# Kernel tuning notes

Hardware: AMD Instinct MI355X
Metric: run time of the kernel (lower is better)

## Reference

```python
import jax, jax.numpy as jnp
import numpy as np

D_IN = 6      # raw node feature dim (self_attn_init first arg)
D_INIT = 16   # init encoding dim (self_attn_init second arg)
D_CAT = 22    # 6 + 16 (self_attn_enc first arg)
D_ENC = 64    # encoding dim (self_attn_enc second arg / gated_aggr_attn)
N = 1024      # number of nodes in node_cloud


def setup_inputs() -> dict:
    key = jax.random.key(0)
    ks = jax.random.split(key, 8)
    return {
        "node_cloud": jax.random.normal(ks[0], (N, D_IN), jnp.float32),
        "Wq_i": jax.random.normal(ks[1], (D_IN, D_INIT), jnp.float32) / np.sqrt(D_IN),
        "Wk_i": jax.random.normal(ks[2], (D_IN, D_INIT), jnp.float32) / np.sqrt(D_IN),
        "Wv_i": jax.random.normal(ks[3], (D_IN, D_INIT), jnp.float32) / np.sqrt(D_IN),
        "Wq_e": jax.random.normal(ks[4], (D_IN, D_ENC), jnp.float32) / np.sqrt(D_IN),
        "Wk_e": jax.random.normal(ks[5], (D_CAT, D_ENC), jnp.float32) / np.sqrt(D_CAT),
        "Wv_e": jax.random.normal(ks[6], (D_CAT, D_ENC), jnp.float32) / np.sqrt(D_CAT),
        "wg": jax.random.normal(ks[7], (D_ENC,), jnp.float32) / np.sqrt(D_ENC),
        "bg": jnp.zeros((), jnp.float32),
    }


def reference(node_cloud, Wq_i, Wk_i, Wv_i, Wq_e, Wk_e, Wv_e, wg, bg):
    # Stage 1: self_attn_init, batched over all C=N centres at once.
    # Per centre c: attend over every node, per-node 16-d encoding.
    Q_i = node_cloud @ Wq_i                     # [C, 16] (one query per centre)
    K_i = node_cloud @ Wk_i                     # [N, 16]
    V_i = node_cloud @ Wv_i                     # [N, 16]
    scores_i = (Q_i @ K_i.T) / np.sqrt(D_INIT)  # [C, N]
    a_i = jax.nn.softmax(scores_i, axis=-1)     # [C, N]
    nce_init = a_i[:, :, None] * V_i[None]      # [C, N, 16]

    # Stage 2: self_attn_enc on concat(raw node feats, init encodings).
    x = jnp.concatenate(
        [jnp.broadcast_to(node_cloud[None], (N, N, D_IN)), nce_init], axis=-1
    )                                            # [C, N, 22]
    Q_e = node_cloud @ Wq_e                      # [C, 64]
    K_e = jnp.einsum("cnf,fd->cnd", x, Wk_e)     # [C, N, 64]
    V_e = jnp.einsum("cnf,fd->cnd", x, Wv_e)     # [C, N, 64]
    scores_e = jnp.einsum("cnd,cd->cn", K_e, Q_e) / np.sqrt(D_ENC)  # [C, N]
    a_e = jax.nn.softmax(scores_e, axis=-1)      # [C, N]
    enc = a_e[:, :, None] * V_e                  # [C, N, 64]

    # Stage 3: gated_aggr_attn over the node axis -> one 64-vector per centre.
    g = jax.nn.sigmoid(enc @ wg + bg)            # [C, N]
    out = jnp.einsum("cn,cnd->cd", g, enc)       # [C, 64]
    return out
```

## Files before the change

kernel.cpp:

```cpp
#include <hip/hip_runtime.h>
#include <math.h>

#define NN 1024
#define DIN 6
#define DI 16
#define DE 64
#define DCAT 22
#define GC 4
#define NTC 512
#define NWAVE (NTC/64)

#define OFF_XT    0
#define OFF_VIT   (OFF_XT + 6*NN)
#define OFF_GR    (OFF_VIT + 16*NN)
#define OFF_GV    (OFF_GR + NN)
#define OFF_QREC  (OFF_GV + NN)

__device__ __forceinline__ float wave_sum(float v) {
    int t;
    t = __builtin_amdgcn_update_dpp(0, __float_as_int(v), 0x111, 0xf, 0xf, true); v += __int_as_float(t);
    t = __builtin_amdgcn_update_dpp(0, __float_as_int(v), 0x112, 0xf, 0xf, true); v += __int_as_float(t);
    t = __builtin_amdgcn_update_dpp(0, __float_as_int(v), 0x114, 0xf, 0xf, true); v += __int_as_float(t);
    t = __builtin_amdgcn_update_dpp(0, __float_as_int(v), 0x118, 0xf, 0xf, true); v += __int_as_float(t);
    t = __builtin_amdgcn_update_dpp(0, __float_as_int(v), 0x142, 0xf, 0xf, true); v += __int_as_float(t);
    t = __builtin_amdgcn_update_dpp(0, __float_as_int(v), 0x143, 0xf, 0xf, true); v += __int_as_float(t);
    return v;
}

__global__ __launch_bounds__(256) void nce_pre(
    const float* __restrict__ nc,
    const float* __restrict__ Wq_i, const float* __restrict__ Wk_i,
    const float* __restrict__ Wv_i, const float* __restrict__ Wq_e,
    const float* __restrict__ Wk_e, const float* __restrict__ Wv_e,
    const float* __restrict__ wg, float* __restrict__ ws)
{
    __shared__ float s_wqi[96], s_wki[96], s_wvi[96];
    __shared__ float s_wqe[384], s_wke[1408], s_wve[1408], s_wg[64];
    __shared__ float s_t[4][64], s_vi[4][16], s_qi[4][16];
    const int tid = threadIdx.x, w = tid >> 6, lane = tid & 63;

    for (int i = tid; i < 96; i += 256) { s_wqi[i]=Wq_i[i]; s_wki[i]=Wk_i[i]; s_wvi[i]=Wv_i[i]; }
    for (int i = tid; i < 384; i += 256) s_wqe[i] = Wq_e[i];
    for (int i = tid; i < 1408; i += 256) { s_wke[i]=Wk_e[i]; s_wve[i]=Wv_e[i]; }
    if (tid < 64) s_wg[tid] = wg[tid];
    __syncthreads();

    const int n = blockIdx.x*4 + w;
    float x[6];
    #pragma unroll
    for (int f = 0; f < 6; ++f) x[f] = nc[n*6 + f];

    float t = 0.f, vr = 0.f;
    #pragma unroll
    for (int f = 0; f < 6; ++f) {
        t  += x[f]*s_wqe[f*64 + lane];
        vr += x[f]*s_wve[f*64 + lane];
    }
    s_t[w][lane] = t;
    if (lane < 16) {
        float vi = 0.f, qi = 0.f;
        #pragma unroll
        for (int f = 0; f < 6; ++f) {
            vi += x[f]*s_wvi[f*16 + lane];
            qi += x[f]*s_wqi[f*16 + lane];
        }
        s_vi[w][lane] = vi; s_qi[w][lane] = qi;
        ws[OFF_VIT + lane*NN + n] = vi;
    }
    __syncthreads();

    float vv = 0.f;
    #pragma unroll
    for (int j = 0; j < 16; ++j) vv += s_vi[w][j]*s_wve[(6+j)*64 + lane];

    float gr = wave_sum(vr*s_wg[lane]);
    float gv = wave_sum(vv*s_wg[lane]);
    if (lane == 63) { ws[OFF_GR + n] = gr; ws[OFF_GV + n] = gv; }

    if (lane < 6) {
        ws[OFF_XT + lane*NN + n] = x[lane];
        float a = 0.f;
        #pragma unroll
        for (int j = 0; j < 16; ++j) a += s_wki[lane*16 + j]*s_qi[w][j];
        ws[OFF_QREC + lane*NN + n] = a*0.25f;
    }
    if (lane < 22) {
        const float* row = s_wke + lane*64;
        float a = 0.f;
        for (int d = 0; d < 64; ++d) a += row[d]*s_t[w][d];
        const int krow = (lane < 6) ? (8 + lane) : (10 + lane);
        ws[OFF_QREC + krow*NN + n] = a*0.125f;
    }
}

__global__ __launch_bounds__(NTC, 2) void nce_centre(
    const float* __restrict__ ws, const float* __restrict__ bgp,
    const float* __restrict__ Wv_e, float* __restrict__ out)
{
    __shared__ float  s_wve[DCAT*DE];
    __shared__ float  s_q[GC][32];
    __shared__ float4 s_red1[NWAVE], s_red2[NWAVE];
    __shared__ float4 s_acc[NWAVE][22];
    __shared__ float  s_fin[22*4];

    const int tid = threadIdx.x, wave = tid >> 6, lane = tid & 63;
    const int c0 = blockIdx.x*GC;

    for (int i = tid; i < DCAT*DE; i += NTC) s_wve[i] = Wv_e[i];
    if (tid < GC*32) s_q[tid >> 5][tid & 31] = ws[OFF_QREC + (tid & 31)*NN + c0 + (tid >> 5)];

    const int nA = tid, nB = tid + NTC;
    float xA[6], xB[6], viA[16], viB[16];
    #pragma unroll
    for (int f = 0; f < 6; ++f) { xA[f] = ws[OFF_XT + f*NN + nA]; xB[f] = ws[OFF_XT + f*NN + nB]; }
    #pragma unroll
    for (int j = 0; j < 16; ++j) { viA[j] = ws[OFF_VIT + j*NN + nA]; viB[j] = ws[OFF_VIT + j*NN + nB]; }
    const float grA = ws[OFF_GR + nA], grB = ws[OFF_GR + nB];
    const float gvA = ws[OFF_GV + nA], gvB = ws[OFF_GV + nB];
    const float bg = *bgp;
    __syncthreads();

    float aiA[GC], aiB[GC];
    {
        float r[GC];
        #pragma unroll
        for (int c = 0; c < GC; ++c) {
            const float* q = s_q[c];
            float sA = 0.f, sB = 0.f;
            #pragma unroll
            for (int f = 0; f < 6; ++f) { sA += q[f]*xA[f]; sB += q[f]*xB[f]; }
            aiA[c] = __expf(sA); aiB[c] = __expf(sB);
            r[c] = aiA[c] + aiB[c];
        }
        float r0 = wave_sum(r[0]), r1 = wave_sum(r[1]), r2 = wave_sum(r[2]), r3 = wave_sum(r[3]);
        if (lane == 63) s_red1[wave] = make_float4(r0, r1, r2, r3);
    }
    __syncthreads();
    {
        float4 dd = s_red1[0];
        #pragma unroll
        for (int w2 = 1; w2 < NWAVE; ++w2) {
            float4 t = s_red1[w2]; dd.x += t.x; dd.y += t.y; dd.z += t.z; dd.w += t.w;
        }
        float den[GC] = {dd.x, dd.y, dd.z, dd.w};
        #pragma unroll
        for (int c = 0; c < GC; ++c) { float inv = 1.f/den[c]; aiA[c] *= inv; aiB[c] *= inv; }
    }

    float w1A[GC], w2A[GC], w1B[GC], w2B[GC];
    {
        float eA[GC], eB[GC];
        #pragma unroll
        for (int c = 0; c < GC; ++c) {
            const float* q = s_q[c];
            float uA = 0.f, uB = 0.f, vA = 0.f, vB = 0.f;
            #pragma unroll
            for (int f = 0; f < 6; ++f) { uA += q[8+f]*xA[f]; uB += q[8+f]*xB[f]; }
            #pragma unroll
            for (int j = 0; j < 16; ++j) { vA += q[16+j]*viA[j]; vB += q[16+j]*viB[j]; }
            eA[c] = __expf(uA + aiA[c]*vA);
            eB[c] = __expf(uB + aiB[c]*vB);
        }
        float s0 = wave_sum(eA[0]+eB[0]), s1 = wave_sum(eA[1]+eB[1]);
        float s2 = wave_sum(eA[2]+eB[2]), s3 = wave_sum(eA[3]+eB[3]);
        if (lane == 63) s_red2[wave] = make_float4(s0, s1, s2, s3);
        __syncthreads();
        float4 dd = s_red2[0];
        #pragma unroll
        for (int w2 = 1; w2 < NWAVE; ++w2) {
            float4 t = s_red2[w2]; dd.x += t.x; dd.y += t.y; dd.z += t.z; dd.w += t.w;
        }
        float den2[GC] = {dd.x, dd.y, dd.z, dd.w};
        #pragma unroll
        for (int c = 0; c < GC; ++c) {
            float inv = 1.f/den2[c];
            float aeA = eA[c]*inv, aeB = eB[c]*inv;
            float preA = aeA*(grA + aiA[c]*gvA) + bg;
            float preB = aeB*(grB + aiB[c]*gvB) + bg;
            float gA = 1.f/(1.f + __expf(-preA));
            float gB = 1.f/(1.f + __expf(-preB));
            w1A[c] = gA*aeA; w2A[c] = w1A[c]*aiA[c];
            w1B[c] = gB*aeB; w2B[c] = w1B[c]*aiB[c];
        }
    }

    #pragma unroll
    for (int f = 0; f < 6; ++f) {
        float a0 = wave_sum(w1A[0]*xA[f] + w1B[0]*xB[f]);
        float a1 = wave_sum(w1A[1]*xA[f] + w1B[1]*xB[f]);
        float a2 = wave_sum(w1A[2]*xA[f] + w1B[2]*xB[f]);
        float a3 = wave_sum(w1A[3]*xA[f] + w1B[3]*xB[f]);
        if (lane == 63) s_acc[wave][f] = make_float4(a0, a1, a2, a3);
    }
    #pragma unroll
    for (int j = 0; j < 16; ++j) {
        float a0 = wave_sum(w2A[0]*viA[j] + w2B[0]*viB[j]);
        float a1 = wave_sum(w2A[1]*viA[j] + w2B[1]*viB[j]);
        float a2 = wave_sum(w2A[2]*viA[j] + w2B[2]*viB[j]);
        float a3 = wave_sum(w2A[3]*viA[j] + w2B[3]*viB[j]);
        if (lane == 63) s_acc[wave][6+j] = make_float4(a0, a1, a2, a3);
    }
    __syncthreads();
    if (tid < 88) {
        const int k = tid >> 2, c = tid & 3;
        const float* af = (const float*)s_acc;
        float a = 0.f;
        #pragma unroll
        for (int w2 = 0; w2 < NWAVE; ++w2) a += af[(w2*22 + k)*4 + c];
        s_fin[k*4 + c] = a;
    }
    __syncthreads();

    if (tid < GC*DE) {
        const int c = tid >> 6, d = tid & 63;
        float o = 0.f;
        #pragma unroll
        for (int k = 0; k < DCAT; ++k) o += s_fin[k*4 + c]*s_wve[k*64 + d];
        out[(c0 + c)*DE + d] = o;
    }
}

extern "C" void kernel_launch(void* const* d_in, const int* in_sizes, int n_in,
                              void* d_out, int out_size, void* d_ws, size_t ws_size,
                              hipStream_t stream)
{
    const float* nc   = (const float*)d_in[0];
    const float* Wq_i = (const float*)d_in[1];
    const float* Wk_i = (const float*)d_in[2];
    const float* Wv_i = (const float*)d_in[3];
    const float* Wq_e = (const float*)d_in[4];
    const float* Wk_e = (const float*)d_in[5];
    const float* Wv_e = (const float*)d_in[6];
    const float* wg   = (const float*)d_in[7];
    const float* bg   = (const float*)d_in[8];
    float* out = (float*)d_out;
    float* ws  = (float*)d_ws;

    nce_pre<<<NN/4, 256, 0, stream>>>(nc, Wq_i, Wk_i, Wv_i, Wq_e, Wk_e, Wv_e, wg, ws);
    nce_centre<<<NN/GC, NTC, 0, stream>>>(ws, bg, Wv_e, out);
}
```

Baseline: 19.33 us.

## Fold weight products into small matrices in single-block setup; halve centres per block

The setup kernel now runs as a single 1024-thread block. It first builds the folded 6x22 matrix Wq_e·Wk_eᵀ, the 6x6 matrix Wq_i·Wk_iᵀ and the vector Wv_e·wg, then computes each node's per-node projections with a few small dot products instead of per-wave 64-wide reductions. The centre kernel handles 2 centres per block instead of 4, which doubles the grid to 512 blocks, and raises the occupancy hint to 4 blocks per CU. This cuts the redundant weight-matrix work in the prologue and spreads the main kernel across more CUs. In exchange, the setup kernel runs on one CU, and every centre block reloads the shared weights and node data twice as often in total.

```diff
diff --git a/kernel.cpp b/kernel.cpp
--- a/kernel.cpp
+++ b/kernel.cpp
@@ -2,19 +2,18 @@
 #include <math.h>
 
 #define NN 1024
-#define DIN 6
-#define DI 16
 #define DE 64
 #define DCAT 22
-#define GC 4
+#define GC 2
 #define NTC 512
 #define NWAVE (NTC/64)
-
-#define OFF_XT    0
-#define OFF_VIT   (OFF_XT + 6*NN)
-#define OFF_GR    (OFF_VIT + 16*NN)
-#define OFF_GV    (OFF_GR + NN)
-#define OFF_QREC  (OFF_GV + NN)
+#define NBLK (NN/GC)
+
+#define OFF_XT   0
+#define OFF_VIT  (OFF_XT + 6*NN)
+#define OFF_GR   (OFF_VIT + 16*NN)
+#define OFF_GV   (OFF_GR + NN)
+#define OFF_QREC (OFF_GV + NN)
 
 __device__ __forceinline__ float wave_sum(float v) {
     int t;
@@ -27,7 +26,7 @@
     return v;
 }
 
-__global__ __launch_bounds__(256) void nce_pre(
+__global__ __launch_bounds__(1024) void nce_setup(
     const float* __restrict__ nc,
     const float* __restrict__ Wq_i, const float* __restrict__ Wk_i,
     const float* __restrict__ Wv_i, const float* __restrict__ Wq_e,
@@ -36,72 +35,83 @@
 {
     __shared__ float s_wqi[96], s_wki[96], s_wvi[96];
     __shared__ float s_wqe[384], s_wke[1408], s_wve[1408], s_wg[64];
-    __shared__ float s_t[4][64], s_vi[4][16], s_qi[4][16];
-    const int tid = threadIdx.x, w = tid >> 6, lane = tid & 63;
-
-    for (int i = tid; i < 96; i += 256) { s_wqi[i]=Wq_i[i]; s_wki[i]=Wk_i[i]; s_wvi[i]=Wv_i[i]; }
-    for (int i = tid; i < 384; i += 256) s_wqe[i] = Wq_e[i];
-    for (int i = tid; i < 1408; i += 256) { s_wke[i]=Wk_e[i]; s_wve[i]=Wv_e[i]; }
-    if (tid < 64) s_wg[tid] = wg[tid];
-    __syncthreads();
-
-    const int n = blockIdx.x*4 + w;
+    __shared__ float s_M[6*DCAT], s_Mi[36], s_u[DCAT];
+    const int tid = threadIdx.x;
+
+    if (tid < 96) { s_wqi[tid]=Wq_i[tid]; s_wki[tid]=Wk_i[tid]; s_wvi[tid]=Wv_i[tid]; }
+    { int t = tid - 128; if (t >= 0 && t < 384) s_wqe[t] = Wq_e[t]; }
+    { int t = tid - 512; if (t >= 0 && t < 64)  s_wg[t]  = wg[t]; }
+    for (int i = tid; i < 1408; i += 1024) { s_wke[i]=Wk_e[i]; s_wve[i]=Wv_e[i]; }
+    __syncthreads();
+
+    if (tid < 132) {
+        const int f = tid % 6, k = tid / 6;
+        float a = 0.f;
+        #pragma unroll
+        for (int d = 0; d < 64; ++d) a += s_wqe[f*64+d]*s_wke[k*64+d];
+        s_M[f*DCAT+k] = a * 0.125f;
+    } else if (tid < 168) {
+        const int t = tid - 132, g = t % 6, f = t / 6;
+        float a = 0.f;
+        #pragma unroll
+        for (int j = 0; j < 16; ++j) a += s_wqi[g*16+j]*s_wki[f*16+j];
+        s_Mi[g*6+f] = a * 0.25f;
+    } else if (tid < 190) {
+        const int k = tid - 168;
+        float a = 0.f;
+        #pragma unroll
+        for (int d = 0; d < 64; ++d) a += s_wve[k*64+d]*s_wg[d];
+        s_u[k] = a;
+    }
+    __syncthreads();
+
+    const int n = tid;
     float x[6];
     #pragma unroll
-    for (int f = 0; f < 6; ++f) x[f] = nc[n*6 + f];
-
-    float t = 0.f, vr = 0.f;
+    for (int f = 0; f < 6; ++f) { x[f] = nc[n*6 + f]; ws[OFF_XT + f*NN + n] = x[f]; }
+
+    float vi[16];
+    #pragma unroll
+    for (int j = 0; j < 16; ++j) {
+        float a = 0.f;
+        #pragma unroll
+        for (int f = 0; f < 6; ++f) a += x[f]*s_wvi[f*16+j];
+        vi[j] = a;
+        ws[OFF_VIT + j*NN + n] = a;
+    }
+    float gr = 0.f, gv = 0.f;
+    #pragma unroll
+    for (int f = 0; f < 6; ++f)  gr += x[f]*s_u[f];
+    #pragma unroll
+    for (int j = 0; j < 16; ++j) gv += vi[j]*s_u[6+j];
+    ws[OFF_GR + n] = gr;
+    ws[OFF_GV + n] = gv;
+
     #pragma unroll
     for (int f = 0; f < 6; ++f) {
-        t  += x[f]*s_wqe[f*64 + lane];
-        vr += x[f]*s_wve[f*64 + lane];
-    }
-    s_t[w][lane] = t;
-    if (lane < 16) {
-        float vi = 0.f, qi = 0.f;
-        #pragma unroll
-        for (int f = 0; f < 6; ++f) {
-            vi += x[f]*s_wvi[f*16 + lane];
-            qi += x[f]*s_wqi[f*16 + lane];
-        }
-        s_vi[w][lane] = vi; s_qi[w][lane] = qi;
-        ws[OFF_VIT + lane*NN + n] = vi;
-    }
-    __syncthreads();
-
-    float vv = 0.f;
-    #pragma unroll
-    for (int j = 0; j < 16; ++j) vv += s_vi[w][j]*s_wve[(6+j)*64 + lane];
-
-    float gr = wave_sum(vr*s_wg[lane]);
-    float gv = wave_sum(vv*s_wg[lane]);
-    if (lane == 63) { ws[OFF_GR + n] = gr; ws[OFF_GV + n] = gv; }
-
-    if (lane < 6) {
-        ws[OFF_XT + lane*NN + n] = x[lane];
-        float a = 0.f;
-        #pragma unroll
-        for (int j = 0; j < 16; ++j) a += s_wki[lane*16 + j]*s_qi[w][j];
-        ws[OFF_QREC + lane*NN + n] = a*0.25f;
-    }
-    if (lane < 22) {
-        const float* row = s_wke + lane*64;
-        float a = 0.f;
-        for (int d = 0; d < 64; ++d) a += row[d]*s_t[w][d];
-        const int krow = (lane < 6) ? (8 + lane) : (10 + lane);
-        ws[OFF_QREC + krow*NN + n] = a*0.125f;
-    }
-}
-
-__global__ __launch_bounds__(NTC, 2) void nce_centre(
+        float a = 0.f;
+        #pragma unroll
+        for (int g = 0; g < 6; ++g) a += x[g]*s_Mi[g*6+f];
+        ws[OFF_QREC + f*NN + n] = a;
+    }
+    #pragma unroll
+    for (int k = 0; k < DCAT; ++k) {
+        float a = 0.f;
+        #pragma unroll
+        for (int f = 0; f < 6; ++f) a += x[f]*s_M[f*DCAT+k];
+        ws[OFF_QREC + ((k < 6) ? (8+k) : (10+k))*NN + n] = a;
+    }
+}
+
+__global__ __launch_bounds__(NTC, 4) void nce_centre(
     const float* __restrict__ ws, const float* __restrict__ bgp,
     const float* __restrict__ Wv_e, float* __restrict__ out)
 {
     __shared__ float  s_wve[DCAT*DE];
     __shared__ float  s_q[GC][32];
-    __shared__ float4 s_red1[NWAVE], s_red2[NWAVE];
-    __shared__ float4 s_acc[NWAVE][22];
-    __shared__ float  s_fin[22*4];
+    __shared__ float2 s_red1[NWAVE], s_red2[NWAVE];
+    __shared__ float2 s_acc[NWAVE][DCAT];
+    __shared__ float  s_fin[DCAT*GC];
 
     const int tid = threadIdx.x, wave = tid >> 6, lane = tid & 63;
     const int c0 = blockIdx.x*GC;
@@ -121,30 +131,26 @@
     __syncthreads();
 
     float aiA[GC], aiB[GC];
+    #pragma unroll
+    for (int c = 0; c < GC; ++c) {
+        const float* q = s_q[c];
+        float sA = 0.f, sB = 0.f;
+        #pragma unroll
+        for (int f = 0; f < 6; ++f) { sA += q[f]*xA[f]; sB += q[f]*xB[f]; }
+        aiA[c] = __expf(sA); aiB[c] = __expf(sB);
+    }
     {
-        float r[GC];
-        #pragma unroll
-        for (int c = 0; c < GC; ++c) {
-            const float* q = s_q[c];
-            float sA = 0.f, sB = 0.f;
-            #pragma unroll
-            for (int f = 0; f < 6; ++f) { sA += q[f]*xA[f]; sB += q[f]*xB[f]; }
-            aiA[c] = __expf(sA); aiB[c] = __expf(sB);
-            r[c] = aiA[c] + aiB[c];
-        }
-        float r0 = wave_sum(r[0]), r1 = wave_sum(r[1]), r2 = wave_sum(r[2]), r3 = wave_sum(r[3]);
-        if (lane == 63) s_red1[wave] = make_float4(r0, r1, r2, r3);
+        float r0 = wave_sum(aiA[0]+aiB[0]);
+        float r1 = wave_sum(aiA[1]+aiB[1]);
+        if (lane == 63) s_red1[wave] = make_float2(r0, r1);
     }
     __syncthreads();
     {
-        float4 dd = s_red1[0];
-        #pragma unroll
-        for (int w2 = 1; w2 < NWAVE; ++w2) {
-            float4 t = s_red1[w2]; dd.x += t.x; dd.y += t.y; dd.z += t.z; dd.w += t.w;
-        }
-        float den[GC] = {dd.x, dd.y, dd.z, dd.w};
-        #pragma unroll
-        for (int c = 0; c < GC; ++c) { float inv = 1.f/den[c]; aiA[c] *= inv; aiB[c] *= inv; }
+        float2 dd = s_red1[0];
+        #pragma unroll
+        for (int w2 = 1; w2 < NWAVE; ++w2) { float2 t = s_red1[w2]; dd.x += t.x; dd.y += t.y; }
+        float inv0 = 1.f/dd.x, inv1 = 1.f/dd.y;
+        aiA[0] *= inv0; aiB[0] *= inv0; aiA[1] *= inv1; aiB[1] *= inv1;
     }
 
     float w1A[GC], w2A[GC], w1B[GC], w2B[GC];
@@ -161,19 +167,17 @@
             eA[c] = __expf(uA + aiA[c]*vA);
             eB[c] = __expf(uB + aiB[c]*vB);
         }
-        float s0 = wave_sum(eA[0]+eB[0]), s1 = wave_sum(eA[1]+eB[1]);
-        float s2 = wave_sum(eA[2]+eB[2]), s3 = wave_sum(eA[3]+eB[3]);
-        if (lane == 63) s_red2[wave] = make_float4(s0, s1, s2, s3);
+        float s0 = wave_sum(eA[0]+eB[0]);
+        float s1 = wave_sum(eA[1]+eB[1]);
+        if (lane == 63) s_red2[wave] = make_float2(s0, s1);
         __syncthreads();
-        float4 dd = s_red2[0];
-        #pragma unroll
-        for (int w2 = 1; w2 < NWAVE; ++w2) {
-            float4 t = s_red2[w2]; dd.x += t.x; dd.y += t.y; dd.z += t.z; dd.w += t.w;
-        }
-        float den2[GC] = {dd.x, dd.y, dd.z, dd.w};
+        float2 dd = s_red2[0];
+        #pragma unroll
+        for (int w2 = 1; w2 < NWAVE; ++w2) { float2 t = s_red2[w2]; dd.x += t.x; dd.y += t.y; }
+        float den[GC] = {dd.x, dd.y};
         #pragma unroll
         for (int c = 0; c < GC; ++c) {
-            float inv = 1.f/den2[c];
+            float inv = 1.f/den[c];
             float aeA = eA[c]*inv, aeB = eB[c]*inv;
             float preA = aeA*(grA + aiA[c]*gvA) + bg;
             float preB = aeB*(grB + aiB[c]*gvB) + bg;
@@ -188,26 +192,22 @@
     for (int f = 0; f < 6; ++f) {
         float a0 = wave_sum(w1A[0]*xA[f] + w1B[0]*xB[f]);
         float a1 = wave_sum(w1A[1]*xA[f] + w1B[1]*xB[f]);
-        float a2 = wave_sum(w1A[2]*xA[f] + w1B[2]*xB[f]);
-        float a3 = wave_sum(w1A[3]*xA[f] + w1B[3]*xB[f]);
-        if (lane == 63) s_acc[wave][f] = make_float4(a0, a1, a2, a3);
+        if (lane == 63) s_acc[wave][f] = make_float2(a0, a1);
     }
     #pragma unroll
     for (int j = 0; j < 16; ++j) {
         float a0 = wave_sum(w2A[0]*viA[j] + w2B[0]*viB[j]);
         float a1 = wave_sum(w2A[1]*viA[j] + w2B[1]*viB[j]);
-        float a2 = wave_sum(w2A[2]*viA[j] + w2B[2]*viB[j]);
-        float a3 = wave_sum(w2A[3]*viA[j] + w2B[3]*viB[j]);
-        if (lane == 63) s_acc[wave][6+j] = make_float4(a0, a1, a2, a3);
-    }
-    __syncthreads();
-    if (tid < 88) {
-        const int k = tid >> 2, c = tid & 3;
-        const float* af = (const float*)s_acc;
-        float a = 0.f;
-        #pragma unroll
-        for (int w2 = 0; w2 < NWAVE; ++w2) a += af[(w2*22 + k)*4 + c];
-        s_fin[k*4 + c] = a;
+        if (lane == 63) s_acc[wave][6+j] = make_float2(a0, a1);
+    }
+    __syncthreads();
+    if (tid < DCAT*GC) {
+        const int k = tid >> 1, c = tid & 1;
+        float a = 0.f;
+        #pragma unroll
+        for (int w2 = 0; w2 < NWAVE; ++w2)
+            a += ((const float*)&s_acc[w2][k])[c];
+        s_fin[k*GC + c] = a;
     }
     __syncthreads();
 
@@ -215,7 +215,7 @@
         const int c = tid >> 6, d = tid & 63;
         float o = 0.f;
         #pragma unroll
-        for (int k = 0; k < DCAT; ++k) o += s_fin[k*4 + c]*s_wve[k*64 + d];
+        for (int k = 0; k < DCAT; ++k) o += s_fin[k*GC + c]*s_wve[k*64 + d];
         out[(c0 + c)*DE + d] = o;
     }
 }
@@ -236,6 +236,6 @@
     float* out = (float*)d_out;
     float* ws  = (float*)d_ws;
 
-    nce_pre<<<NN/4, 256, 0, stream>>>(nc, Wq_i, Wk_i, Wv_i, Wq_e, Wk_e, Wv_e, wg, ws);
-    nce_centre<<<NN/GC, NTC, 0, stream>>>(ws, bg, Wv_e, out);
-}
+    nce_setup<<<1, 1024, 0, stream>>>(nc, Wq_i, Wk_i, Wv_i, Wq_e, Wk_e, Wv_e, wg, ws);
+    nce_centre<<<NBLK, NTC, 0, stream>>>(ws, bg, Wv_e, out);
+}
```

After: 21.38 us. +10.6%, slower.
